# Optimization experiments

Measured on AMD Instinct MI355X. Metric: run time of the kernel, lower is better.

The kernel has to match this reference:

```python
import jax, jax.numpy as jnp
import numpy as np

V, E, U, L = 50000, 512, 20, 9   # vocab, embed dim, user feats, labels
R, S, T = 64, 32, 50             # reviews, sentences/review, tokens/sentence
D = E + U                        # product-encoder input dim


def setup_inputs() -> dict:
    key = jax.random.key(0)
    ks = jax.random.split(key, 16)
    sc = lambda k, shape: (jax.random.normal(k, shape, jnp.float32) * 0.02)
    return {
        "inputs": jax.random.randint(ks[0], (R, S, T), 0, V),
        "user_feats": jax.random.normal(ks[1], (R, U), jnp.float32),
        "embedding": sc(ks[2], (V, E)),
        "w_sent": sc(ks[3], (E, E)), "b_sent": jnp.zeros((E,), jnp.float32),
        "w_rev": sc(ks[4], (E, E)),  "b_rev": jnp.zeros((E,), jnp.float32),
        "w_prod": sc(ks[5], (D, D)), "b_prod": jnp.zeros((D,), jnp.float32),
        "w_rff": sc(ks[6], (D, 1)),  "b_rff": jnp.zeros((1,), jnp.float32),
        "w_pff": sc(ks[7], (D, L)),  "b_pff": jnp.zeros((L,), jnp.float32),
        "user_w": jnp.ones((U,), jnp.float32),
    }


def _masked_mean(x, mask):
    # x: [..., N, F], mask: [..., N] -> [..., F]
    denom = jnp.maximum(mask.sum(-1, keepdims=True), 1.0)
    return (x * mask[..., None]).sum(-2) / denom


def reference(inputs, user_feats, embedding, w_sent, b_sent, w_rev, b_rev,
              w_prod, b_prod, w_rff, b_rff, w_pff, b_pff, user_w):
    dt = embedding.dtype
    tok_mask = (inputs != 0).astype(dt)                      # [R,S,T]
    emb = embedding[inputs]                                  # [R,S,T,E]
    # sentence encoder (DAN): masked mean over tokens + Linear + SELU
    sent_h = jax.nn.selu(_masked_mean(emb, tok_mask) @ w_sent + b_sent)   # [R,S,E]
    # review encoder: masked mean over sentences (r_mask = p.sum(-1) != 0)
    sent_mask = (inputs.sum(-1) != 0).astype(dt)             # [R,S]
    rev_h = jax.nn.selu(_masked_mean(sent_h, sent_mask) @ w_rev + b_rev)  # [R,E]
    # append L2-normalized user feats scaled by learned weights
    norm = jnp.sqrt((user_feats * user_feats).sum(-1, keepdims=True))
    uf = user_feats / jnp.maximum(norm, 1e-12) * user_w      # [R,U]
    p_batch = jnp.concatenate([rev_h, uf], axis=-1)          # [R,D]
    # per-review star head
    r_stars = jax.nn.selu(p_batch @ w_rff + b_rff).squeeze(-1)            # [R]
    # product encoder: plain mean over reviews (no mask) + Linear + SELU
    h_n = jax.nn.selu(p_batch.mean(-2) @ w_prod + b_prod)    # [D]
    p_stars = jax.nn.selu(h_n @ w_pff + b_pff)               # [L]
    return p_stars, r_stars
```

## Files before the change

### kernel.cpp

```cpp
#include <hip/hip_runtime.h>
#include <hip/hip_bf16.h>

#define R_ 64
#define S_ 32
#define T_ 50
#define E_ 512
#define U_ 20
#define D_ 532
#define L_ 9
#define NSENT (R_ * S_)

#define PCHUNK 128
#define NCG 5
#define NKG 5

typedef __attribute__((ext_vector_type(8))) short bf16x8;
typedef __attribute__((ext_vector_type(4))) float f32x4;

__device__ __forceinline__ float selu_f(float x) {
    const float scale = 1.0507009873554805f;
    const float alpha = 1.6732632423543772f;
    return x > 0.0f ? scale * x : scale * alpha * expm1f(x);
}

__device__ __forceinline__ void store_out(float* p, float v) { *p = v; }
__device__ __forceinline__ void store_out(__hip_bfloat16* p, float v) { *p = __float2bfloat16(v); }

__global__ __launch_bounds__(256) void k_fused_A(
        const int* __restrict__ inputs,
        const float* __restrict__ emb,
        const float* __restrict__ w_sent,
        const float* __restrict__ w_rev,
        __hip_bfloat16* __restrict__ sent_bf,
        __hip_bfloat16* __restrict__ wT,
        float* __restrict__ smask)
{
    const int tid = threadIdx.x;

    if (blockIdx.x >= NSENT) {
        __shared__ float tile[32][33];
        const int b = blockIdx.x - NSENT;
        const int z = b >> 8;
        const float* w = z ? w_rev : w_sent;
        __hip_bfloat16* o = wT + (size_t)z * E_ * E_;
        const int bb = b & 255;
        const int tx = tid & 31, ty = tid >> 5;
        const int k0 = (bb >> 4) * 32, n0 = (bb & 15) * 32;
        #pragma unroll
        for (int i = 0; i < 4; ++i)
            tile[ty + 8 * i][tx] = w[(size_t)(k0 + ty + 8 * i) * E_ + n0 + tx];
        __syncthreads();
        #pragma unroll
        for (int i = 0; i < 4; ++i)
            o[(size_t)(n0 + ty + 8 * i) * E_ + k0 + tx] = __float2bfloat16(tile[tx][ty + 8 * i]);
        return;
    }

    const int sid = blockIdx.x;
    const int base = sid * T_;
    float2 acc = {0.f, 0.f};
    int cnt = 0;
    for (int t = 0; t < T_; ++t) {
        const int tok = inputs[base + t];
        const float m = (tok != 0) ? 1.0f : 0.0f;
        cnt += (tok != 0);
        const float2 v = ((const float2*)(emb + (size_t)tok * E_))[tid];
        acc.x = fmaf(v.x, m, acc.x);
        acc.y = fmaf(v.y, m, acc.y);
    }
    const float inv = 1.0f / fmaxf((float)cnt, 1.0f);
    __hip_bfloat162 h2;
    h2.x = __float2bfloat16(acc.x * inv);
    h2.y = __float2bfloat16(acc.y * inv);
    ((__hip_bfloat162*)(sent_bf + (size_t)sid * E_))[tid] = h2;
    if (tid == 0) smask[sid] = (cnt > 0) ? 1.0f : 0.0f;
}

template <typename OutT>
__global__ __launch_bounds__(256) void k_gemm_selu(
        const __hip_bfloat16* __restrict__ A,
        const __hip_bfloat16* __restrict__ Bt,
        const float* __restrict__ bias,
        OutT* __restrict__ C, int ldc)
{
    __shared__ short As[64][40];
    __shared__ short Bs[64][40];
    const int tid  = threadIdx.x;
    const int wid  = tid >> 6;
    const int lane = tid & 63;
    const int wm = wid >> 1, wn = wid & 1;
    const int bm = blockIdx.y * 64, bn = blockIdx.x * 64;

    const int srow = tid >> 2;
    const int soff = (tid & 3) * 8;

    const short* Ag  = (const short*)A;
    const short* Btg = (const short*)Bt;

    f32x4 acc[2][2];
    #pragma unroll
    for (int i = 0; i < 2; ++i)
        #pragma unroll
        for (int j = 0; j < 2; ++j) acc[i][j] = (f32x4){0.f, 0.f, 0.f, 0.f};

    const int fr = lane & 15;
    const int kg = (lane >> 4) * 8;

    for (int k0 = 0; k0 < E_; k0 += 32) {
        __syncthreads();
        *(bf16x8*)&As[srow][soff] = *(const bf16x8*)&Ag[(size_t)(bm + srow) * E_ + k0 + soff];
        *(bf16x8*)&Bs[srow][soff] = *(const bf16x8*)&Btg[(size_t)(bn + srow) * E_ + k0 + soff];
        __syncthreads();
        bf16x8 af0 = *(const bf16x8*)&As[wm * 32 + fr][kg];
        bf16x8 af1 = *(const bf16x8*)&As[wm * 32 + 16 + fr][kg];
        bf16x8 bf0 = *(const bf16x8*)&Bs[wn * 32 + fr][kg];
        bf16x8 bf1 = *(const bf16x8*)&Bs[wn * 32 + 16 + fr][kg];
        acc[0][0] = __builtin_amdgcn_mfma_f32_16x16x32_bf16(af0, bf0, acc[0][0], 0, 0, 0);
        acc[0][1] = __builtin_amdgcn_mfma_f32_16x16x32_bf16(af0, bf1, acc[0][1], 0, 0, 0);
        acc[1][0] = __builtin_amdgcn_mfma_f32_16x16x32_bf16(af1, bf0, acc[1][0], 0, 0, 0);
        acc[1][1] = __builtin_amdgcn_mfma_f32_16x16x32_bf16(af1, bf1, acc[1][1], 0, 0, 0);
    }

    const int rq = (lane >> 4) * 4;
    #pragma unroll
    for (int fm = 0; fm < 2; ++fm) {
        #pragma unroll
        for (int fn = 0; fn < 2; ++fn) {
            const int col = bn + wn * 32 + fn * 16 + fr;
            const float bv = bias[col];
            #pragma unroll
            for (int j = 0; j < 4; ++j) {
                const int row = bm + wm * 32 + fm * 16 + rq + j;
                store_out(&C[(size_t)row * ldc + col], selu_f(acc[fm][fn][j] + bv));
            }
        }
    }
}

__global__ __launch_bounds__(256) void k_rev_mean(
        const __hip_bfloat16* __restrict__ sent_h,
        const float* __restrict__ smask,
        __hip_bfloat16* __restrict__ mrev)
{
    const int r = blockIdx.x;
    const int tid = threadIdx.x;
    float2 acc = {0.f, 0.f};
    float msum = 0.f;
    for (int s = 0; s < S_; ++s) {
        const float m = smask[r * S_ + s];
        const __hip_bfloat162 v = ((const __hip_bfloat162*)(sent_h + (size_t)(r * S_ + s) * E_))[tid];
        acc.x = fmaf(__bfloat162float(v.x), m, acc.x);
        acc.y = fmaf(__bfloat162float(v.y), m, acc.y);
        msum += m;
    }
    const float inv = 1.0f / fmaxf(msum, 1.0f);
    __hip_bfloat162 h2;
    h2.x = __float2bfloat16(acc.x * inv);
    h2.y = __float2bfloat16(acc.y * inv);
    ((__hip_bfloat162*)(mrev + (size_t)r * E_))[tid] = h2;
}

__global__ __launch_bounds__(64) void k_pbatch(
        const float* __restrict__ user_feats,
        const float* __restrict__ user_w,
        const float* __restrict__ w_rff,
        const float* __restrict__ b_rff,
        float* __restrict__ p_batch,
        float* __restrict__ out_r)
{
    __shared__ float uf[U_];
    const int r = blockIdx.x;
    const int tid = threadIdx.x;
    if (tid < U_) {
        float ss = 0.f;
        #pragma unroll
        for (int j = 0; j < U_; ++j) {
            const float u = user_feats[r * U_ + j];
            ss = fmaf(u, u, ss);
        }
        const float nrm = fmaxf(sqrtf(ss), 1e-12f);
        const float v = user_feats[r * U_ + tid] / nrm * user_w[tid];
        uf[tid] = v;
        p_batch[(size_t)r * D_ + E_ + tid] = v;
    }
    __syncthreads();
    float part = 0.f;
    #pragma unroll
    for (int i = 0; i < 8; ++i)
        part = fmaf(p_batch[(size_t)r * D_ + tid + 64 * i], w_rff[tid + 64 * i], part);
    if (tid < U_) part = fmaf(uf[tid], w_rff[E_ + tid], part);
    #pragma unroll
    for (int off = 32; off > 0; off >>= 1) part += __shfl_down(part, off, 64);
    if (tid == 0) out_r[r] = selu_f(part + b_rff[0]);
}

__global__ __launch_bounds__(256) void k_prod_partial(
        const float* __restrict__ p_batch,
        const float* __restrict__ w_prod,
        float* __restrict__ part)
{
    __shared__ float pbar[PCHUNK];
    __shared__ float red[2][PCHUNK];
    const int cg = blockIdx.x, kg = blockIdx.y;
    const int tid = threadIdx.x;
    const int cl = tid & (PCHUNK - 1);
    const int h  = tid >> 7;
    const int k0 = kg * PCHUNK;
    const int klen = min(PCHUNK, D_ - k0);

    if (cl < klen) {
        float s = 0.f;
        #pragma unroll 8
        for (int r = h * 32; r < h * 32 + 32; ++r)
            s += p_batch[(size_t)r * D_ + k0 + cl];
        red[h][cl] = s;
    }
    __syncthreads();
    if (h == 0 && cl < klen) pbar[cl] = (red[0][cl] + red[1][cl]) * (1.0f / 64.0f);
    __syncthreads();

    const int c = cg * PCHUNK + cl;
    float acc = 0.f;
    if (c < D_) {
        const int jb = h * 64;
        const int je = min(jb + 64, klen);
        for (int j = jb; j < je; ++j)
            acc = fmaf(pbar[j], w_prod[(size_t)(k0 + j) * D_ + c], acc);
    }
    red[h][cl] = acc;
    __syncthreads();
    if (h == 0 && c < D_) part[kg * D_ + c] = red[0][cl] + red[1][cl];
}

__global__ __launch_bounds__(256) void k_prod_final(
        const float* __restrict__ part,
        const float* __restrict__ b_prod,
        const float* __restrict__ w_pff,
        const float* __restrict__ b_pff,
        float* __restrict__ out_p)
{
    __shared__ float hn[D_];
    const int tid = threadIdx.x;
    for (int c = tid; c < D_; c += 256) {
        float s = b_prod[c];
        #pragma unroll
        for (int kg = 0; kg < NKG; ++kg) s += part[kg * D_ + c];
        hn[c] = selu_f(s);
    }
    __syncthreads();
    if (tid < L_) {
        float a = 0.f;
        for (int k = 0; k < D_; ++k) a = fmaf(hn[k], w_pff[k * L_ + tid], a);
        out_p[tid] = selu_f(a + b_pff[tid]);
    }
}

extern "C" void kernel_launch(void* const* d_in, const int* in_sizes, int n_in,
                              void* d_out, int out_size, void* d_ws, size_t ws_size,
                              hipStream_t stream) {
    const int*   inputs     = (const int*)  d_in[0];
    const float* user_feats = (const float*)d_in[1];
    const float* emb        = (const float*)d_in[2];
    const float* w_sent     = (const float*)d_in[3];
    const float* b_sent     = (const float*)d_in[4];
    const float* w_rev      = (const float*)d_in[5];
    const float* b_rev      = (const float*)d_in[6];
    const float* w_prod     = (const float*)d_in[7];
    const float* b_prod     = (const float*)d_in[8];
    const float* w_rff      = (const float*)d_in[9];
    const float* b_rff      = (const float*)d_in[10];
    const float* w_pff      = (const float*)d_in[11];
    const float* b_pff      = (const float*)d_in[12];
    const float* user_w     = (const float*)d_in[13];
    float* out = (float*)d_out;

    float* ws = (float*)d_ws;
    __hip_bfloat16* sent_bf  = (__hip_bfloat16*)(ws);
    __hip_bfloat16* sent_hbf = (__hip_bfloat16*)(ws + 524288);
    __hip_bfloat16* wT       = (__hip_bfloat16*)(ws + 1048576);
    __hip_bfloat16* mrev     = (__hip_bfloat16*)(ws + 1310720);
    float* smask   = ws + 1327104;
    float* p_batch = ws + 1329152;
    float* part    = ws + 1363200;

    k_fused_A<<<NSENT + 512, 256, 0, stream>>>(inputs, emb, w_sent, w_rev,
                                               sent_bf, wT, smask);
    k_gemm_selu<__hip_bfloat16><<<dim3(E_ / 64, NSENT / 64), 256, 0, stream>>>(
        sent_bf, wT, b_sent, sent_hbf, E_);
    k_rev_mean<<<R_, 256, 0, stream>>>(sent_hbf, smask, mrev);
    k_gemm_selu<float><<<dim3(E_ / 64, R_ / 64), 256, 0, stream>>>(
        mrev, wT + (size_t)E_ * E_, b_rev, p_batch, D_);
    k_pbatch<<<R_, 64, 0, stream>>>(user_feats, user_w, w_rff, b_rff, p_batch, out + L_);
    k_prod_partial<<<dim3(NCG, NKG), 256, 0, stream>>>(p_batch, w_prod, part);
    k_prod_final<<<1, 256, 0, stream>>>(part, b_prod, w_pff, b_pff, out);
}
```

Before: 80.04 us.

## Fuse sentence-mean into GEMM epilogue and merge tail kernels via last-block atomic

```diff
diff --git a/kernel.cpp b/kernel.cpp
--- a/kernel.cpp
+++ b/kernel.cpp
@@ -23,9 +23,6 @@
     return x > 0.0f ? scale * x : scale * alpha * expm1f(x);
 }
 
-__device__ __forceinline__ void store_out(float* p, float v) { *p = v; }
-__device__ __forceinline__ void store_out(__hip_bfloat16* p, float v) { *p = __float2bfloat16(v); }
-
 __global__ __launch_bounds__(256) void k_fused_A(
         const int* __restrict__ inputs,
         const float* __restrict__ emb,
@@ -33,7 +30,8 @@
         const float* __restrict__ w_rev,
         __hip_bfloat16* __restrict__ sent_bf,
         __hip_bfloat16* __restrict__ wT,
-        float* __restrict__ smask)
+        float* __restrict__ smask,
+        int* __restrict__ dcount)
 {
     const int tid = threadIdx.x;
 
@@ -55,6 +53,8 @@
             o[(size_t)(n0 + ty + 8 * i) * E_ + k0 + tx] = __float2bfloat16(tile[tx][ty + 8 * i]);
         return;
     }
+
+    if (blockIdx.x == 0 && tid == 0) *dcount = 0;
 
     const int sid = blockIdx.x;
     const int base = sid * T_;
@@ -76,12 +76,12 @@
     if (tid == 0) smask[sid] = (cnt > 0) ? 1.0f : 0.0f;
 }
 
-template <typename OutT>
-__global__ __launch_bounds__(256) void k_gemm_selu(
+__global__ __launch_bounds__(256) void k_gemm_sent_mean(
         const __hip_bfloat16* __restrict__ A,
         const __hip_bfloat16* __restrict__ Bt,
         const float* __restrict__ bias,
-        OutT* __restrict__ C, int ldc)
+        const float* __restrict__ smask,
+        __hip_bfloat16* __restrict__ mrev)
 {
     __shared__ short As[64][40];
     __shared__ short Bs[64][40];
@@ -122,6 +122,104 @@
     }
 
     const int rq = (lane >> 4) * 4;
+    float m[2][4];
+    float msum = 0.f;
+    #pragma unroll
+    for (int fm = 0; fm < 2; ++fm)
+        #pragma unroll
+        for (int j = 0; j < 4; ++j) {
+            m[fm][j] = smask[bm + wm * 32 + fm * 16 + rq + j];
+            msum += m[fm][j];
+        }
+    float colsum[2];
+    #pragma unroll
+    for (int fn = 0; fn < 2; ++fn) {
+        const float bv = bias[bn + wn * 32 + fn * 16 + fr];
+        float s = 0.f;
+        #pragma unroll
+        for (int fm = 0; fm < 2; ++fm)
+            #pragma unroll
+            for (int j = 0; j < 4; ++j)
+                s = fmaf(selu_f(acc[fm][fn][j] + bv), m[fm][j], s);
+        colsum[fn] = s;
+    }
+    #pragma unroll
+    for (int fn = 0; fn < 2; ++fn) {
+        colsum[fn] += __shfl_xor(colsum[fn], 16, 64);
+        colsum[fn] += __shfl_xor(colsum[fn], 32, 64);
+    }
+    msum += __shfl_xor(msum, 16, 64);
+    msum += __shfl_xor(msum, 32, 64);
+    const float inv = 1.0f / fmaxf(msum, 1.0f);
+    if (lane < 16) {
+        const int g = 2 * blockIdx.y + wm;
+        #pragma unroll
+        for (int fn = 0; fn < 2; ++fn)
+            mrev[(size_t)g * E_ + bn + wn * 32 + fn * 16 + fr] =
+                __float2bfloat16(colsum[fn] * inv);
+    }
+}
+
+__global__ __launch_bounds__(256) void k_gemm_rev(
+        const __hip_bfloat16* __restrict__ A,
+        const __hip_bfloat16* __restrict__ Bt,
+        const float* __restrict__ bias,
+        const float* __restrict__ user_feats,
+        const float* __restrict__ user_w,
+        float* __restrict__ p_batch)
+{
+    __shared__ short As[64][40];
+    __shared__ short Bs[64][40];
+    const int tid  = threadIdx.x;
+    const int wid  = tid >> 6;
+    const int lane = tid & 63;
+    const int wm = wid >> 1, wn = wid & 1;
+    const int bn = blockIdx.x * 64;
+
+    if (blockIdx.x == 0 && tid < 64) {
+        const int r = tid;
+        float ss = 0.f;
+        #pragma unroll
+        for (int j = 0; j < U_; ++j) {
+            const float u = user_feats[r * U_ + j];
+            ss = fmaf(u, u, ss);
+        }
+        const float nrm = fmaxf(sqrtf(ss), 1e-12f);
+        #pragma unroll
+        for (int j = 0; j < U_; ++j)
+            p_batch[(size_t)r * D_ + E_ + j] = user_feats[r * U_ + j] / nrm * user_w[j];
+    }
+
+    const int srow = tid >> 2;
+    const int soff = (tid & 3) * 8;
+    const short* Ag  = (const short*)A;
+    const short* Btg = (const short*)Bt;
+
+    f32x4 acc[2][2];
+    #pragma unroll
+    for (int i = 0; i < 2; ++i)
+        #pragma unroll
+        for (int j = 0; j < 2; ++j) acc[i][j] = (f32x4){0.f, 0.f, 0.f, 0.f};
+
+    const int fr = lane & 15;
+    const int kg = (lane >> 4) * 8;
+
+    for (int k0 = 0; k0 < E_; k0 += 32) {
+        __syncthreads();
+        *(bf16x8*)&As[srow][soff] = *(const bf16x8*)&Ag[(size_t)srow * E_ + k0 + soff];
+        *(bf16x8*)&Bs[srow][soff] = *(const bf16x8*)&Btg[(size_t)(bn + srow) * E_ + k0 + soff];
+        __syncthreads();
+        bf16x8 af0 = *(const bf16x8*)&As[wm * 32 + fr][kg];
+        bf16x8 af1 = *(const bf16x8*)&As[wm * 32 + 16 + fr][kg];
+        bf16x8 bf0 = *(const bf16x8*)&Bs[wn * 32 + fr][kg];
+        bf16x8 bf1 = *(const bf16x8*)&Bs[wn * 32 + 16 + fr][kg];
+        acc[0][0] = __builtin_amdgcn_mfma_f32_16x16x32_bf16(af0, bf0, acc[0][0], 0, 0, 0);
+        acc[0][1] = __builtin_amdgcn_mfma_f32_16x16x32_bf16(af0, bf1, acc[0][1], 0, 0, 0);
+        acc[1][0] = __builtin_amdgcn_mfma_f32_16x16x32_bf16(af1, bf0, acc[1][0], 0, 0, 0);
+        acc[1][1] = __builtin_amdgcn_mfma_f32_16x16x32_bf16(af1, bf1, acc[1][1], 0, 0, 0);
+    }
+
+    const int rq = (lane >> 4) * 4;
     #pragma unroll
     for (int fm = 0; fm < 2; ++fm) {
         #pragma unroll
@@ -130,74 +228,25 @@
             const float bv = bias[col];
             #pragma unroll
             for (int j = 0; j < 4; ++j) {
-                const int row = bm + wm * 32 + fm * 16 + rq + j;
-                store_out(&C[(size_t)row * ldc + col], selu_f(acc[fm][fn][j] + bv));
+                const int row = wm * 32 + fm * 16 + rq + j;
+                p_batch[(size_t)row * D_ + col] = selu_f(acc[fm][fn][j] + bv);
             }
         }
     }
 }
 
-__global__ __launch_bounds__(256) void k_rev_mean(
-        const __hip_bfloat16* __restrict__ sent_h,
-        const float* __restrict__ smask,
-        __hip_bfloat16* __restrict__ mrev)
-{
-    const int r = blockIdx.x;
-    const int tid = threadIdx.x;
-    float2 acc = {0.f, 0.f};
-    float msum = 0.f;
-    for (int s = 0; s < S_; ++s) {
-        const float m = smask[r * S_ + s];
-        const __hip_bfloat162 v = ((const __hip_bfloat162*)(sent_h + (size_t)(r * S_ + s) * E_))[tid];
-        acc.x = fmaf(__bfloat162float(v.x), m, acc.x);
-        acc.y = fmaf(__bfloat162float(v.y), m, acc.y);
-        msum += m;
-    }
-    const float inv = 1.0f / fmaxf(msum, 1.0f);
-    __hip_bfloat162 h2;
-    h2.x = __float2bfloat16(acc.x * inv);
-    h2.y = __float2bfloat16(acc.y * inv);
-    ((__hip_bfloat162*)(mrev + (size_t)r * E_))[tid] = h2;
-}
-
-__global__ __launch_bounds__(64) void k_pbatch(
-        const float* __restrict__ user_feats,
-        const float* __restrict__ user_w,
+__global__ __launch_bounds__(256) void k_prod_fused(
+        const float* __restrict__ p_batch,
+        const float* __restrict__ w_prod,
+        const float* __restrict__ b_prod,
+        const float* __restrict__ w_pff,
+        const float* __restrict__ b_pff,
         const float* __restrict__ w_rff,
         const float* __restrict__ b_rff,
-        float* __restrict__ p_batch,
+        float* __restrict__ part,
+        int* __restrict__ dcount,
+        float* __restrict__ out_p,
         float* __restrict__ out_r)
-{
-    __shared__ float uf[U_];
-    const int r = blockIdx.x;
-    const int tid = threadIdx.x;
-    if (tid < U_) {
-        float ss = 0.f;
-        #pragma unroll
-        for (int j = 0; j < U_; ++j) {
-            const float u = user_feats[r * U_ + j];
-            ss = fmaf(u, u, ss);
-        }
-        const float nrm = fmaxf(sqrtf(ss), 1e-12f);
-        const float v = user_feats[r * U_ + tid] / nrm * user_w[tid];
-        uf[tid] = v;
-        p_batch[(size_t)r * D_ + E_ + tid] = v;
-    }
-    __syncthreads();
-    float part = 0.f;
-    #pragma unroll
-    for (int i = 0; i < 8; ++i)
-        part = fmaf(p_batch[(size_t)r * D_ + tid + 64 * i], w_rff[tid + 64 * i], part);
-    if (tid < U_) part = fmaf(uf[tid], w_rff[E_ + tid], part);
-    #pragma unroll
-    for (int off = 32; off > 0; off >>= 1) part += __shfl_down(part, off, 64);
-    if (tid == 0) out_r[r] = selu_f(part + b_rff[0]);
-}
-
-__global__ __launch_bounds__(256) void k_prod_partial(
-        const float* __restrict__ p_batch,
-        const float* __restrict__ w_prod,
-        float* __restrict__ part)
 {
     __shared__ float pbar[PCHUNK];
     __shared__ float red[2][PCHUNK];
@@ -230,22 +279,21 @@
     red[h][cl] = acc;
     __syncthreads();
     if (h == 0 && c < D_) part[kg * D_ + c] = red[0][cl] + red[1][cl];
-}
-
-__global__ __launch_bounds__(256) void k_prod_final(
-        const float* __restrict__ part,
-        const float* __restrict__ b_prod,
-        const float* __restrict__ w_pff,
-        const float* __restrict__ b_pff,
-        float* __restrict__ out_p)
-{
+
+    __threadfence();
+    __shared__ int is_last;
+    if (tid == 0) is_last = (atomicAdd(dcount, 1) == NCG * NKG - 1);
+    __syncthreads();
+    if (!is_last) return;
+    __threadfence();
+
     __shared__ float hn[D_];
-    const int tid = threadIdx.x;
-    for (int c = tid; c < D_; c += 256) {
-        float s = b_prod[c];
-        #pragma unroll
-        for (int kg = 0; kg < NKG; ++kg) s += part[kg * D_ + c];
-        hn[c] = selu_f(s);
+    __shared__ float rred[4][64];
+    for (int cc = tid; cc < D_; cc += 256) {
+        float s = b_prod[cc];
+        #pragma unroll
+        for (int g = 0; g < NKG; ++g) s += part[g * D_ + cc];
+        hn[cc] = selu_f(s);
     }
     __syncthreads();
     if (tid < L_) {
@@ -253,6 +301,17 @@
         for (int k = 0; k < D_; ++k) a = fmaf(hn[k], w_pff[k * L_ + tid], a);
         out_p[tid] = selu_f(a + b_pff[tid]);
     }
+    {
+        const int r = tid & 63, q = tid >> 6;
+        float pr = 0.f;
+        for (int k = q * 133; k < (q + 1) * 133; ++k)
+            pr = fmaf(p_batch[(size_t)r * D_ + k], w_rff[k], pr);
+        rred[q][r] = pr;
+    }
+    __syncthreads();
+    if (tid < 64)
+        out_r[tid] = selu_f(rred[0][tid] + rred[1][tid] + rred[2][tid] + rred[3][tid]
+                            + b_rff[0]);
 }
 
 extern "C" void kernel_launch(void* const* d_in, const int* in_sizes, int n_in,
@@ -275,22 +334,21 @@
     float* out = (float*)d_out;
 
     float* ws = (float*)d_ws;
-    __hip_bfloat16* sent_bf  = (__hip_bfloat16*)(ws);
-    __hip_bfloat16* sent_hbf = (__hip_bfloat16*)(ws + 524288);
-    __hip_bfloat16* wT       = (__hip_bfloat16*)(ws + 1048576);
-    __hip_bfloat16* mrev     = (__hip_bfloat16*)(ws + 1310720);
-    float* smask   = ws + 1327104;
-    float* p_batch = ws + 1329152;
-    float* part    = ws + 1363200;
+    __hip_bfloat16* sent_bf = (__hip_bfloat16*)(ws);
+    __hip_bfloat16* wT      = (__hip_bfloat16*)(ws + 524288);
+    __hip_bfloat16* mrev    = (__hip_bfloat16*)(ws + 786432);
+    float* smask   = ws + 802816;
+    float* p_batch = ws + 804864;
+    float* part    = ws + 838912;
+    int*   dcount  = (int*)(ws + 841600);
 
     k_fused_A<<<NSENT + 512, 256, 0, stream>>>(inputs, emb, w_sent, w_rev,
-                                               sent_bf, wT, smask);
-    k_gemm_selu<__hip_bfloat16><<<dim3(E_ / 64, NSENT / 64), 256, 0, stream>>>(
-        sent_bf, wT, b_sent, sent_hbf, E_);
-    k_rev_mean<<<R_, 256, 0, stream>>>(sent_hbf, smask, mrev);
-    k_gemm_selu<float><<<dim3(E_ / 64, R_ / 64), 256, 0, stream>>>(
-        mrev, wT + (size_t)E_ * E_, b_rev, p_batch, D_);
-    k_pbatch<<<R_, 64, 0, stream>>>(user_feats, user_w, w_rff, b_rff, p_batch, out + L_);
-    k_prod_partial<<<dim3(NCG, NKG), 256, 0, stream>>>(p_batch, w_prod, part);
-    k_prod_final<<<1, 256, 0, stream>>>(part, b_prod, w_pff, b_pff, out);
-}
+                                               sent_bf, wT, smask, dcount);
+    k_gemm_sent_mean<<<dim3(E_ / 64, NSENT / 64), 256, 0, stream>>>(
+        sent_bf, wT, b_sent, smask, mrev);
+    k_gemm_rev<<<dim3(E_ / 64, 1), 256, 0, stream>>>(
+        mrev, wT + (size_t)E_ * E_, b_rev, user_feats, user_w, p_batch);
+    k_prod_fused<<<dim3(NCG, NKG), 256, 0, stream>>>(
+        p_batch, w_prod, b_prod, w_pff, b_pff, w_rff, b_rff,
+        part, dcount, out, out + L_);
+}
```

New measurement: 81.31 us. About the same (+1.6%).
